# Performance work log

Hardware: AMD Instinct MI355X
Metric: run time of the kernel (lower is better)

The kernel has to match this reference:

```python
import jax, jax.numpy as jnp
import numpy as np

P = 16  # patch_size


def _tokenize(x, p):
    # (B,C,H,W) -> (B,C,nP,p,p), row-major patch order
    B, C, H, W = x.shape
    nH, nW = H // p, W // p
    x = x.reshape(B, C, nH, p, nW, p).transpose(0, 1, 2, 4, 3, 5)
    return x.reshape(B, C, nH * nW, p, p)


def _untokenize(t, p, H, W):
    B, C, nP, _, _ = t.shape
    nH, nW = H // p, W // p
    t = t.reshape(B, C, nH, nW, p, p).transpose(0, 1, 2, 4, 3, 5)
    return t.reshape(B, C, H, W)


def _sinusoidal_pe(n, d):
    pos = jnp.arange(n, dtype=jnp.float32)[:, None]                    # (n,1)
    div = jnp.exp(jnp.arange(0, d, 2, dtype=jnp.float32) * (-jnp.log(10000.0) / d))
    ang = pos * div                                                     # (n, d/2)
    pe = jnp.zeros((n, d), dtype=jnp.float32)
    pe = pe.at[:, 0::2].set(jnp.sin(ang))
    pe = pe.at[:, 1::2].set(jnp.cos(ang)[:, : d // 2])
    return pe


def setup_inputs() -> dict:
    key = jax.random.key(0)
    ks = jax.random.split(key, 7)
    B, C, H, W = 16, 3, 512, 512
    nh = 12
    D = C * P * P            # 768 token dim
    dh = D // nh             # 64 head dim
    s = 0.02
    x = jax.random.normal(ks[0], (B, C, H, W), dtype=jnp.float32)
    Wq = jax.random.normal(ks[1], (nh, D, dh), dtype=jnp.float32) * s
    Wk = jax.random.normal(ks[2], (nh, D, dh), dtype=jnp.float32) * s
    Wv = jax.random.normal(ks[3], (nh, D, dh), dtype=jnp.float32) * s
    bq = jax.random.normal(ks[4], (nh, dh), dtype=jnp.float32) * s
    bk = jax.random.normal(ks[5], (nh, dh), dtype=jnp.float32) * s
    bv = jax.random.normal(ks[6], (nh, dh), dtype=jnp.float32) * s
    return {"x": x, "Wq": Wq, "bq": bq, "Wk": Wk, "bk": bk, "Wv": Wv, "bv": bv}


def reference(x, Wq, bq, Wk, bk, Wv, bv):
    B, C, H, W = x.shape
    nh, D, dh = Wq.shape
    tok = _tokenize(x, P)                      # (B,C,nP,p,p)
    nP = tok.shape[2]
    t = tok.reshape(B, nP, D)                  # torch .view semantics (row-major reshape)
    pe = _sinusoidal_pe(nP, D)
    t = 2.0 * t + pe[None]
    # batched per-head projections (H heads, independent weights)
    q = jnp.einsum('bnd,hde->bhne', t, Wq) + bq[None, :, None, :]
    k = jnp.einsum('bnd,hde->bhne', t, Wk) + bk[None, :, None, :]
    v = jnp.einsum('bnd,hde->bhne', t, Wv) + bv[None, :, None, :]
    scores = jnp.einsum('bhne,bhme->bhnm', q, k) / jnp.sqrt(jnp.float32(dh))
    attn = jax.nn.softmax(scores, axis=-1)
    o = jnp.einsum('bhnm,bhme->bhne', attn, v)  # (B,nh,nP,dh)
    # concat heads along last dim
    out = o.transpose(0, 2, 1, 3).reshape(B, nP, D)
    out = out.reshape(B, C, nP, P, P)          # torch .view back
    return _untokenize(out, P, H, W)
```

## Files before the change

### kernel.cpp

```cpp
#include <hip/hip_runtime.h>
#include <hip/hip_bf16.h>
#include <math.h>

typedef short bf16x8 __attribute__((ext_vector_type(8)));
typedef float f32x4 __attribute__((ext_vector_type(4)));

static __device__ __forceinline__ unsigned short f2bf(float f) {
  unsigned int u = __float_as_uint(f);
  u += 0x7FFFu + ((u >> 16) & 1u);
  return (unsigned short)(u >> 16);
}

static __device__ __forceinline__ void gload16(const unsigned short* g, unsigned short* l) {
  __builtin_amdgcn_global_load_lds(
      (const __attribute__((address_space(1))) unsigned int*)g,
      (__attribute__((address_space(3))) unsigned int*)l, 16, 0, 0);
}

__global__ __launch_bounds__(256) void k_prep_w(const float* __restrict__ Wq,
                                                const float* __restrict__ Wk,
                                                const float* __restrict__ Wv,
                                                unsigned short* __restrict__ wt) {
  __shared__ unsigned short lw[64][72];
  int sh = blockIdx.x;
  int kt = blockIdx.y;
  int s = sh / 12, h = sh - s * 12;
  const float* W = (s == 0 ? Wq : (s == 1 ? Wk : Wv)) + h * 49152 + (kt << 6) * 64;
  int tid = threadIdx.x;
#pragma unroll
  for (int it = 0; it < 4; ++it) {
    int idx = it * 256 + tid;
    int kk = idx >> 4, e4 = (idx & 15) << 2;
    float4 v = *(const float4*)(W + kk * 64 + e4);
    lw[e4 + 0][kk] = f2bf(v.x);
    lw[e4 + 1][kk] = f2bf(v.y);
    lw[e4 + 2][kk] = f2bf(v.z);
    lw[e4 + 3][kk] = f2bf(v.w);
  }
  __syncthreads();
  unsigned short* outp = wt + sh * 49152 + (kt << 6);
#pragma unroll
  for (int it = 0; it < 2; ++it) {
    int c = it * 256 + tid;
    int e = c >> 3, kc = (c & 7) << 3;
    *(uint4*)(outp + e * 768 + kc) = *(const uint4*)&lw[e][kc];
  }
}

__global__ __launch_bounds__(256) void k_build_t(const float* __restrict__ x,
                                                 unsigned short* __restrict__ t) {
  int g = blockIdx.x * 256 + threadIdx.x;
  int f = g << 3;
  int m  = f / 768;
  int d  = f - m * 768;
  int c  = f >> 18;
  int rl = f & 262143;
  int n  = rl >> 8;
  int qq = rl & 255;
  int ii = qq >> 4, jj = qq & 15;
  float pe8[8];
#pragma unroll
  for (int u = 0; u < 8; ++u) {
    int dd = d + u;
    int k = dd >> 1;
    float ang = (float)m * expf(-0.023985261385f * (float)k);
    pe8[u] = (dd & 1) ? cosf(ang) : sinf(ang);
  }
  const float* xp0 = x + (c << 18) + (((n >> 5) << 4) + ii) * 512 + ((n & 31) << 4) + jj;
  for (int b = 0; b < 16; ++b) {
    const float* xp = xp0 + b * 786432;
    float4 v0 = *(const float4*)xp;
    float4 v1 = *(const float4*)(xp + 4);
    float xv[8] = {v0.x, v0.y, v0.z, v0.w, v1.x, v1.y, v1.z, v1.w};
    unsigned short tmp[8];
#pragma unroll
    for (int u = 0; u < 8; ++u) tmp[u] = f2bf(2.0f * xv[u] + pe8[u]);
    *(uint4*)(t + b * 786432 + f) = *(const uint4*)tmp;
  }
}

union SMQ {
  struct { unsigned short A[128][32]; unsigned short B[128][32]; } g;
  unsigned short tr[64][136];
};
__global__ __launch_bounds__(256) void k_qkv(
    const unsigned short* __restrict__ t, const unsigned short* __restrict__ wt,
    const float* __restrict__ bq, const float* __restrict__ bk, const float* __restrict__ bv,
    unsigned short* __restrict__ qout, unsigned short* __restrict__ kout,
    unsigned short* __restrict__ vout) {
  __shared__ SMQ sm;
  int bid = blockIdx.x;
  int xcd = bid & 7, idx = bid >> 3;
  int rt = xcd * 16 + idx / 18;
  int jt = idx % 18;
  int row0 = rt << 7;
  int j0 = jt << 7;
  int s = jt / 6;
  int h0 = (jt % 6) * 2;
  const float* bias = (s == 0 ? bq : (s == 1 ? bk : bv));
  unsigned short* outp = (s == 0 ? qout : (s == 1 ? kout : vout));
  int tid = threadIdx.x, lane = tid & 63, w = tid >> 6;
  int wm = w >> 1, wn = w & 1;
  int g = lane >> 4, q16 = lane & 15;
  const unsigned short* gA0 = t  + (row0 + 32 * w + (lane >> 2)) * 768 + ((lane & 3) << 3);
  const unsigned short* gA1 = gA0 + 16 * 768;
  const unsigned short* gB0 = wt + (j0 + 32 * w + (lane >> 2)) * 768 + ((lane & 3) << 3);
  const unsigned short* gB1 = gB0 + 16 * 768;
  unsigned short* lA0 = &sm.g.A[32 * w][0];
  unsigned short* lA1 = &sm.g.A[32 * w + 16][0];
  unsigned short* lB0 = &sm.g.B[32 * w][0];
  unsigned short* lB1 = &sm.g.B[32 * w + 16][0];
  f32x4 acc[4][4] = {};
  for (int k0 = 0; k0 < 768; k0 += 32) {
    __syncthreads();
    gload16(gA0 + k0, lA0);
    gload16(gA1 + k0, lA1);
    gload16(gB0 + k0, lB0);
    gload16(gB1 + k0, lB1);
    __syncthreads();
    bf16x8 a[4], b[4];
#pragma unroll
    for (int mi = 0; mi < 4; ++mi)
      a[mi] = *(const bf16x8*)&sm.g.A[wm * 64 + mi * 16 + q16][g << 3];
#pragma unroll
    for (int ni = 0; ni < 4; ++ni)
      b[ni] = *(const bf16x8*)&sm.g.B[wn * 64 + ni * 16 + q16][g << 3];
#pragma unroll
    for (int mi = 0; mi < 4; ++mi)
#pragma unroll
      for (int ni = 0; ni < 4; ++ni)
        acc[mi][ni] = __builtin_amdgcn_mfma_f32_16x16x32_bf16(a[mi], b[ni], acc[mi][ni], 0, 0, 0);
  }
  int bb2 = row0 >> 10, n0 = row0 & 1023;
  if (s < 2) {
    float qs = (s == 0) ? 0.18033688011f : 1.0f;
#pragma unroll
    for (int ni = 0; ni < 4; ++ni) {
      int colg = wn * 64 + ni * 16 + q16;
      int h = h0 + (colg >> 6);
      int e = colg & 63;
      float be = bias[h * 64 + e];
      int base = (bb2 * 12 + h) << 16;
#pragma unroll
      for (int mi = 0; mi < 4; ++mi)
#pragma unroll
        for (int r = 0; r < 4; ++r) {
          int n = n0 + wm * 64 + mi * 16 + (g << 2) + r;
          outp[base + (n << 6) + e] = f2bf((acc[mi][ni][r] + be) * qs);
        }
    }
  } else {
#pragma unroll
    for (int hh = 0; hh < 2; ++hh) {
      __syncthreads();
      if (wn == hh) {
#pragma unroll
        for (int ni = 0; ni < 4; ++ni) {
          int e = ni * 16 + q16;
          float be = bias[(h0 + hh) * 64 + e];
#pragma unroll
          for (int mi = 0; mi < 4; ++mi)
#pragma unroll
            for (int rp = 0; rp < 2; ++rp) {
              int rr = (wm * 2 + (mi >> 1)) * 32 + g * 8 + (mi & 1) * 4 + rp * 2;
              unsigned int lo = f2bf(acc[mi][ni][rp * 2] + be);
              unsigned int hi = f2bf(acc[mi][ni][rp * 2 + 1] + be);
              *(unsigned int*)&sm.tr[e][rr] = lo | (hi << 16);
            }
        }
      }
      __syncthreads();
      int base = (bb2 * 12 + h0 + hh) << 16;
#pragma unroll
      for (int it = 0; it < 4; ++it) {
        int c = it * 256 + tid;
        int e = c >> 4, nc = (c & 15) << 3;
        *(uint4*)(vout + base + (e << 10) + n0 + nc) = *(const uint4*)&sm.tr[e][nc];
      }
    }
  }
}

__global__ __launch_bounds__(256) void k_attn(
    const unsigned short* __restrict__ Q,
    const unsigned short* __restrict__ K,
    const unsigned short* __restrict__ Vg,
    float* __restrict__ out) {
  __shared__ unsigned short Kt[64][72];
  __shared__ unsigned short Vt[80][72];
  int bid = blockIdx.x;
  int xcd = bid & 7, idx = bid >> 3;
  int bh = xcd * 24 + (idx >> 3);
  int qt = idx & 7;
  int b = bh / 12, h = bh - b * 12;
  int tid = threadIdx.x, lane = tid & 63, w = tid >> 6;
  int g = lane >> 4, q16 = lane & 15;
  int base = bh << 16;
  const unsigned short* Qp = Q + base + (qt << 7) * 64;
  const unsigned short* Kp = K + base;
  const unsigned short* Vp = Vg + base;
  {
    int rr = 64 + (tid >> 4), c4 = (tid & 15) << 2;
    ushort4 z = {0, 0, 0, 0};
    if ((tid >> 4) == 0) { z.x = z.y = z.z = z.w = 0x3F80; }
    *(ushort4*)&Vt[rr][c4] = z;
  }
  bf16x8 qa[2][2];
#pragma unroll
  for (int mt = 0; mt < 2; ++mt)
#pragma unroll
    for (int kf = 0; kf < 2; ++kf)
      qa[mt][kf] = *(const bf16x8*)(Qp + (w * 32 + mt * 16 + q16) * 64 + kf * 32 + (g << 3));
  f32x4 o[2][5] = {};
  float mrow[2] = {-1e30f, -1e30f};
  for (int kv0 = 0; kv0 < 1024; kv0 += 64) {
    __syncthreads();
#pragma unroll
    for (int it = 0; it < 2; ++it) {
      int idx2 = it * 256 + tid;
      int rr = idx2 >> 3, cc = (idx2 & 7) << 3;
      *(uint4*)&Kt[rr][cc] = *(const uint4*)(Kp + (kv0 << 6) + (idx2 << 3));
      *(uint4*)&Vt[rr][cc] = *(const uint4*)(Vp + (rr << 10) + kv0 + cc);
    }
    __syncthreads();
    f32x4 s[2][4] = {};
#pragma unroll
    for (int cb = 0; cb < 4; ++cb) {
      bf16x8 ka0 = *(const bf16x8*)&Kt[cb * 16 + q16][g << 3];
      bf16x8 ka1 = *(const bf16x8*)&Kt[cb * 16 + q16][32 + (g << 3)];
#pragma unroll
      for (int mt = 0; mt < 2; ++mt) {
        s[mt][cb] = __builtin_amdgcn_mfma_f32_16x16x32_bf16(ka0, qa[mt][0], s[mt][cb], 0, 0, 0);
        s[mt][cb] = __builtin_amdgcn_mfma_f32_16x16x32_bf16(ka1, qa[mt][1], s[mt][cb], 0, 0, 0);
      }
    }
    float pmax[2];
#pragma unroll
    for (int mt = 0; mt < 2; ++mt) {
      float mx = s[mt][0][0];
#pragma unroll
      for (int cb = 0; cb < 4; ++cb)
#pragma unroll
        for (int r = 0; r < 4; ++r) mx = fmaxf(mx, s[mt][cb][r]);
      mx = fmaxf(mx, __shfl_xor(mx, 16));
      mx = fmaxf(mx, __shfl_xor(mx, 32));
      pmax[mt] = mx;
    }
    if (__any((pmax[0] > mrow[0] + 8.f) || (pmax[1] > mrow[1] + 8.f))) {
#pragma unroll
      for (int mt = 0; mt < 2; ++mt) {
        float mnew = fmaxf(mrow[mt], pmax[mt]);
        float sc = __builtin_amdgcn_exp2f(mrow[mt] - mnew);
        mrow[mt] = mnew;
#pragma unroll
        for (int r = 0; r < 4; ++r) {
          float scr = __shfl(sc, (g << 2) + r);
#pragma unroll
          for (int cb = 0; cb < 5; ++cb) o[mt][cb][r] *= scr;
        }
      }
    }
    unsigned int pk[2][4][2];
#pragma unroll
    for (int mt = 0; mt < 2; ++mt)
#pragma unroll
      for (int cb = 0; cb < 4; ++cb)
#pragma unroll
        for (int j2 = 0; j2 < 2; ++j2) {
          float plo = __builtin_amdgcn_exp2f(s[mt][cb][2 * j2] - mrow[mt]);
          float phi = __builtin_amdgcn_exp2f(s[mt][cb][2 * j2 + 1] - mrow[mt]);
          asm("v_cvt_pk_bf16_f32 %0, %1, %2" : "=v"(pk[mt][cb][j2]) : "v"(plo), "v"(phi));
        }
#pragma unroll
    for (int kk = 0; kk < 2; ++kk) {
      union { unsigned int u[4]; bf16x8 v; } pa[2];
#pragma unroll
      for (int mt = 0; mt < 2; ++mt) {
        pa[mt].u[0] = pk[mt][2 * kk][0];
        pa[mt].u[1] = pk[mt][2 * kk][1];
        pa[mt].u[2] = pk[mt][2 * kk + 1][0];
        pa[mt].u[3] = pk[mt][2 * kk + 1][1];
      }
#pragma unroll
      for (int cb = 0; cb < 5; ++cb) {
        bf16x8 vb = *(const bf16x8*)&Vt[cb * 16 + q16][kk * 32 + (g << 3)];
#pragma unroll
        for (int mt = 0; mt < 2; ++mt)
          o[mt][cb] = __builtin_amdgcn_mfma_f32_16x16x32_bf16(pa[mt].v, vb, o[mt][cb], 0, 0, 0);
      }
    }
  }
#pragma unroll
  for (int mt = 0; mt < 2; ++mt)
#pragma unroll
    for (int r = 0; r < 4; ++r) {
      float lr = __shfl(o[mt][4][r], lane & 48);
      float inv = 1.0f / lr;
      int m = (qt << 7) + w * 32 + mt * 16 + (g << 2) + r;
#pragma unroll
      for (int cb = 0; cb < 4; ++cb) {
        int d = (h << 6) + cb * 16 + q16;
        int f = m * 768 + d;
        int c = f >> 18, rl = f & 262143, n = rl >> 8, qq = rl & 255;
        out[((b * 3 + c) << 18) + (((n >> 5) << 4) + (qq >> 4)) * 512 + ((n & 31) << 4) + (qq & 15)] =
            o[mt][cb][r] * inv;
      }
    }
}

extern "C" void kernel_launch(void* const* d_in, const int* in_sizes, int n_in,
                              void* d_out, int out_size, void* d_ws, size_t ws_size,
                              hipStream_t stream) {
  const float* x  = (const float*)d_in[0];
  const float* Wq = (const float*)d_in[1];
  const float* bq = (const float*)d_in[2];
  const float* Wk = (const float*)d_in[3];
  const float* bk = (const float*)d_in[4];
  const float* Wv = (const float*)d_in[5];
  const float* bv = (const float*)d_in[6];
  float* out = (float*)d_out;
  unsigned short* wt = (unsigned short*)d_ws;
  unsigned short* t  = wt + 1769472;
  unsigned short* qw = t  + 12582912;
  unsigned short* kw = qw + 12582912;
  unsigned short* vw = kw + 12582912;
  k_prep_w<<<dim3(36, 12), 256, 0, stream>>>(Wq, Wk, Wv, wt);
  k_build_t<<<384, 256, 0, stream>>>(x, t);
  k_qkv<<<2304, 256, 0, stream>>>(t, wt, bq, bk, bv, qw, kw, vw);
  k_attn<<<1536, 256, 0, stream>>>(qw, kw, vw, out);
}
```

Before: 206.7 us.

## Double-buffer LDS in QKV GEMM and precompute positional encoding table

```diff
diff --git a/kernel.cpp b/kernel.cpp
--- a/kernel.cpp
+++ b/kernel.cpp
@@ -47,25 +47,38 @@
   }
 }
 
+__global__ __launch_bounds__(256) void k_pe(unsigned short* __restrict__ pe) {
+  int g = blockIdx.x * 256 + threadIdx.x;
+  int f = g << 3;
+  int m = f / 768;
+  int d = f - m * 768;
+  unsigned short tmp[8];
+#pragma unroll
+  for (int u = 0; u < 8; ++u) {
+    int dd = d + u;
+    int k = dd >> 1;
+    float ang = (float)m * expf(-0.023985261385f * (float)k);
+    tmp[u] = f2bf((dd & 1) ? cosf(ang) : sinf(ang));
+  }
+  *(uint4*)(pe + f) = *(const uint4*)tmp;
+}
+
 __global__ __launch_bounds__(256) void k_build_t(const float* __restrict__ x,
+                                                 const unsigned short* __restrict__ pe,
                                                  unsigned short* __restrict__ t) {
   int g = blockIdx.x * 256 + threadIdx.x;
   int f = g << 3;
-  int m  = f / 768;
-  int d  = f - m * 768;
   int c  = f >> 18;
   int rl = f & 262143;
   int n  = rl >> 8;
   int qq = rl & 255;
   int ii = qq >> 4, jj = qq & 15;
-  float pe8[8];
-#pragma unroll
-  for (int u = 0; u < 8; ++u) {
-    int dd = d + u;
-    int k = dd >> 1;
-    float ang = (float)m * expf(-0.023985261385f * (float)k);
-    pe8[u] = (dd & 1) ? cosf(ang) : sinf(ang);
-  }
+  uint4 peu = *(const uint4*)(pe + f);
+  unsigned int pw[4] = {peu.x, peu.y, peu.z, peu.w};
+  float pef[8];
+#pragma unroll
+  for (int u = 0; u < 8; ++u)
+    pef[u] = __uint_as_float(((pw[u >> 1] >> ((u & 1) * 16)) & 0xFFFFu) << 16);
   const float* xp0 = x + (c << 18) + (((n >> 5) << 4) + ii) * 512 + ((n & 31) << 4) + jj;
   for (int b = 0; b < 16; ++b) {
     const float* xp = xp0 + b * 786432;
@@ -74,15 +87,27 @@
     float xv[8] = {v0.x, v0.y, v0.z, v0.w, v1.x, v1.y, v1.z, v1.w};
     unsigned short tmp[8];
 #pragma unroll
-    for (int u = 0; u < 8; ++u) tmp[u] = f2bf(2.0f * xv[u] + pe8[u]);
+    for (int u = 0; u < 8; ++u) tmp[u] = f2bf(2.0f * xv[u] + pef[u]);
     *(uint4*)(t + b * 786432 + f) = *(const uint4*)tmp;
   }
 }
 
 union SMQ {
-  struct { unsigned short A[128][32]; unsigned short B[128][32]; } g;
+  struct { unsigned short A[2][128][32]; unsigned short B[2][128][32]; } g;
   unsigned short tr[64][136];
 };
+#define QKV_STEP(BUF)                                                                   \
+  {                                                                                     \
+    bf16x8 a[4], b[4];                                                                  \
+    _Pragma("unroll") for (int mi = 0; mi < 4; ++mi)                                    \
+        a[mi] = *(const bf16x8*)&sm.g.A[BUF][wm * 64 + mi * 16 + q16][g << 3];          \
+    _Pragma("unroll") for (int ni = 0; ni < 4; ++ni)                                    \
+        b[ni] = *(const bf16x8*)&sm.g.B[BUF][wn * 64 + ni * 16 + q16][g << 3];          \
+    _Pragma("unroll") for (int mi = 0; mi < 4; ++mi)                                    \
+        _Pragma("unroll") for (int ni = 0; ni < 4; ++ni)                                \
+            acc[mi][ni] =                                                               \
+                __builtin_amdgcn_mfma_f32_16x16x32_bf16(a[mi], b[ni], acc[mi][ni], 0, 0, 0); \
+  }
 __global__ __launch_bounds__(256) void k_qkv(
     const unsigned short* __restrict__ t, const unsigned short* __restrict__ wt,
     const float* __restrict__ bq, const float* __restrict__ bk, const float* __restrict__ bv,
@@ -106,30 +131,34 @@
   const unsigned short* gA1 = gA0 + 16 * 768;
   const unsigned short* gB0 = wt + (j0 + 32 * w + (lane >> 2)) * 768 + ((lane & 3) << 3);
   const unsigned short* gB1 = gB0 + 16 * 768;
-  unsigned short* lA0 = &sm.g.A[32 * w][0];
-  unsigned short* lA1 = &sm.g.A[32 * w + 16][0];
-  unsigned short* lB0 = &sm.g.B[32 * w][0];
-  unsigned short* lB1 = &sm.g.B[32 * w + 16][0];
+  unsigned short* lA0b0 = &sm.g.A[0][32 * w][0];
+  unsigned short* lA1b0 = &sm.g.A[0][32 * w + 16][0];
+  unsigned short* lB0b0 = &sm.g.B[0][32 * w][0];
+  unsigned short* lB1b0 = &sm.g.B[0][32 * w + 16][0];
+  unsigned short* lA0b1 = &sm.g.A[1][32 * w][0];
+  unsigned short* lA1b1 = &sm.g.A[1][32 * w + 16][0];
+  unsigned short* lB0b1 = &sm.g.B[1][32 * w][0];
+  unsigned short* lB1b1 = &sm.g.B[1][32 * w + 16][0];
   f32x4 acc[4][4] = {};
-  for (int k0 = 0; k0 < 768; k0 += 32) {
+  gload16(gA0, lA0b0); gload16(gA1, lA1b0);
+  gload16(gB0, lB0b0); gload16(gB1, lB1b0);
+  asm volatile("s_waitcnt vmcnt(0)" ::: "memory");
+  __syncthreads();
+  for (int k0 = 0; k0 < 768; k0 += 64) {
+    if (k0 + 32 < 768) {
+      gload16(gA0 + k0 + 32, lA0b1); gload16(gA1 + k0 + 32, lA1b1);
+      gload16(gB0 + k0 + 32, lB0b1); gload16(gB1 + k0 + 32, lB1b1);
+    }
+    QKV_STEP(0);
+    asm volatile("s_waitcnt vmcnt(0)" ::: "memory");
     __syncthreads();
-    gload16(gA0 + k0, lA0);
-    gload16(gA1 + k0, lA1);
-    gload16(gB0 + k0, lB0);
-    gload16(gB1 + k0, lB1);
+    if (k0 + 64 < 768) {
+      gload16(gA0 + k0 + 64, lA0b0); gload16(gA1 + k0 + 64, lA1b0);
+      gload16(gB0 + k0 + 64, lB0b0); gload16(gB1 + k0 + 64, lB1b0);
+    }
+    QKV_STEP(1);
+    asm volatile("s_waitcnt vmcnt(0)" ::: "memory");
     __syncthreads();
-    bf16x8 a[4], b[4];
-#pragma unroll
-    for (int mi = 0; mi < 4; ++mi)
-      a[mi] = *(const bf16x8*)&sm.g.A[wm * 64 + mi * 16 + q16][g << 3];
-#pragma unroll
-    for (int ni = 0; ni < 4; ++ni)
-      b[ni] = *(const bf16x8*)&sm.g.B[wn * 64 + ni * 16 + q16][g << 3];
-#pragma unroll
-    for (int mi = 0; mi < 4; ++mi)
-#pragma unroll
-      for (int ni = 0; ni < 4; ++ni)
-        acc[mi][ni] = __builtin_amdgcn_mfma_f32_16x16x32_bf16(a[mi], b[ni], acc[mi][ni], 0, 0, 0);
   }
   int bb2 = row0 >> 10, n0 = row0 & 1023;
   if (s < 2) {
@@ -324,8 +353,10 @@
   unsigned short* qw = t  + 12582912;
   unsigned short* kw = qw + 12582912;
   unsigned short* vw = kw + 12582912;
+  unsigned short* pe = qw;
+  k_pe<<<384, 256, 0, stream>>>(pe);
   k_prep_w<<<dim3(36, 12), 256, 0, stream>>>(Wq, Wk, Wv, wt);
-  k_build_t<<<384, 256, 0, stream>>>(x, t);
+  k_build_t<<<384, 256, 0, stream>>>(x, pe, t);
   k_qkv<<<2304, 256, 0, stream>>>(t, wt, bq, bk, bv, qw, kw, vw);
   k_attn<<<1536, 256, 0, stream>>>(qw, kw, vw, out);
 }
```

After: 204.7 us. No clear change (-0.9%).
